# Kernel tuning notes

Hardware: AMD Instinct MI355X
Metric: run time of the kernel (lower is better)

## Reference

```python
import jax, jax.numpy as jnp
import numpy as np
import math

B, C, H, W = 8, 64, 64, 64


def setup_inputs() -> dict:
    key = jax.random.key(0)
    k1, k2, k3, k4 = jax.random.split(key, 4)
    x = jax.random.normal(k1, (B, C, H, W), dtype=jnp.float32)
    fg_mask = jax.random.randint(k2, (B, 1, H, W), 0, 2, dtype=jnp.int32)
    w_qkv = jax.random.normal(k3, (3 * C, C), dtype=jnp.float32) * (1.0 / math.sqrt(C))
    w_proj = jax.random.normal(k4, (C, C), dtype=jnp.float32) * (1.0 / math.sqrt(C))
    b_proj = jnp.zeros((C,), dtype=jnp.float32)
    return {"x": x, "fg_mask": fg_mask, "w_qkv": w_qkv, "w_proj": w_proj, "b_proj": b_proj}


def reference(x, fg_mask, w_qkv, w_proj, b_proj):
    b, c, h, w = x.shape
    n = h * w
    # [B,C,H,W] -> [B,N,C]
    x_flat = x.reshape(b, c, n).transpose(0, 2, 1)
    qkv = x_flat @ w_qkv.T                      # [B,N,3C]
    q, k, v = jnp.split(qkv, 3, axis=-1)        # each [B,N,C]
    attn = jnp.einsum('bnc,bmc->bnm', q, k) / math.sqrt(c)  # [B,N,N]
    fg = fg_mask.reshape(b, n)                  # [B,N]
    attn = jnp.where(fg[:, None, :] == 0, -jnp.inf, attn)
    attn = jax.nn.softmax(attn, axis=-1)
    out = attn @ v                              # [B,N,C]
    out = out @ w_proj.T + b_proj               # [B,N,C]
    return out.transpose(0, 2, 1).reshape(b, c, h, w)
```

## Files before the change

kernel.cpp:

```cpp
#include <hip/hip_runtime.h>
#include <math.h>

#define Bdim 8
#define Cdim 64
#define Ndim 4096
#define TK   32
#define GNT  32

typedef __bf16 bf16x8 __attribute__((ext_vector_type(8)));
typedef __bf16 bf16x4 __attribute__((ext_vector_type(4)));
typedef float  f32x4  __attribute__((ext_vector_type(4)));
typedef float  f32x16 __attribute__((ext_vector_type(16)));

__device__ __forceinline__ void gload_lds16(const void* g, void* l) {
    __builtin_amdgcn_global_load_lds(
        (const __attribute__((address_space(1))) void*)g,
        (__attribute__((address_space(3))) void*)l, 16, 0, 0);
}

__device__ __forceinline__ float fexp2(float x) {
#if __has_builtin(__builtin_amdgcn_exp2f)
    return __builtin_amdgcn_exp2f(x);
#else
    return exp2f(x);
#endif
}

__global__ __launch_bounds__(256) void qkv_mfma_kernel(
    const float* __restrict__ x, const float* __restrict__ w_qkv,
    const int* __restrict__ fg,
    __bf16* __restrict__ Qb, __bf16* __restrict__ Kb, __bf16* __restrict__ Vb,
    float* __restrict__ fgb)
{
    __shared__ __align__(16) __bf16 whs[64 * 64];
    __shared__ __align__(16) __bf16 wls[64 * 64];
    __shared__ __align__(16) __bf16 tr[4][16 * 64];

    const int bx   = blockIdx.x;
    const int jc   = bx % 3;
    const int nblk = (bx / 3) & 63;
    const int b    = bx / 192;
    const int tid  = threadIdx.x;
    const int wv   = tid >> 6;
    const int l    = tid & 63;
    const int g    = l >> 4;
    const int li   = l & 15;
    const int nbase = nblk * 64 + wv * 16;

    const float KS = 0.125f * 1.44269504089f;

    if (jc == 1 && tid < 64) {
        const int n = nblk * 64 + tid;
        fgb[b * Ndim + n] = fg[b * Ndim + n] ? -12.f : -1e30f;
    }

    {
        const float* wsrc = w_qkv + jc * 4096 + tid * 16;
        const float4 f0 = *(const float4*)(wsrc);
        const float4 f1 = *(const float4*)(wsrc + 4);
        const float4 f2 = *(const float4*)(wsrc + 8);
        const float4 f3 = *(const float4*)(wsrc + 12);
        const int row = tid >> 2;
        const int gb  = (tid & 3) * 2;
        bf16x8 h0, l0, h1, l1;
        const float* fp[4] = {(const float*)&f0, (const float*)&f1,
                              (const float*)&f2, (const float*)&f3};
#pragma unroll
        for (int qq = 0; qq < 2; ++qq)
#pragma unroll
            for (int e = 0; e < 8; ++e) {
                const float v = fp[qq * 2 + (e >> 2)][e & 3];
                const __bf16 h = (__bf16)v;
                if (qq == 0) { h0[e] = h; l0[e] = (__bf16)(v - (float)h); }
                else         { h1[e] = h; l1[e] = (__bf16)(v - (float)h); }
            }
        *(bf16x8*)(whs + row * 64 + 8 * ((gb)     ^ (row & 7))) = h0;
        *(bf16x8*)(whs + row * 64 + 8 * ((gb + 1) ^ (row & 7))) = h1;
        *(bf16x8*)(wls + row * 64 + 8 * ((gb)     ^ (row & 7))) = l0;
        *(bf16x8*)(wls + row * 64 + 8 * ((gb + 1) ^ (row & 7))) = l1;
    }

    bf16x8 xhi[2], xlo[2];
#pragma unroll
    for (int kc = 0; kc < 2; ++kc)
#pragma unroll
        for (int jj = 0; jj < 8; ++jj) {
            const int c = kc * 32 + 8 * g + jj;
            const float v = x[((size_t)(b * 64 + c)) * Ndim + nbase + li];
            const __bf16 h = (__bf16)v;
            xhi[kc][jj] = h;
            xlo[kc][jj] = (__bf16)(v - (float)h);
        }
    __syncthreads();

    __bf16* trw = tr[wv];
    const float qs = (jc == 0) ? KS : 1.f;

#pragma unroll
    for (int jt = 0; jt < 4; ++jt) {
        const int rw = 16 * jt + li;
        const int rs = li & 7;
        const bf16x8 ah0 = *(const bf16x8*)(whs + rw * 64 + 8 * (g ^ rs));
        const bf16x8 ah1 = *(const bf16x8*)(whs + rw * 64 + 8 * ((4 + g) ^ rs));
        const bf16x8 al0 = *(const bf16x8*)(wls + rw * 64 + 8 * (g ^ rs));
        const bf16x8 al1 = *(const bf16x8*)(wls + rw * 64 + 8 * ((4 + g) ^ rs));
        f32x4 d = (f32x4){0.f, 0.f, 0.f, 0.f};
        d = __builtin_amdgcn_mfma_f32_16x16x32_bf16(ah0, xhi[0], d, 0, 0, 0);
        d = __builtin_amdgcn_mfma_f32_16x16x32_bf16(ah1, xhi[1], d, 0, 0, 0);
        d = __builtin_amdgcn_mfma_f32_16x16x32_bf16(ah0, xlo[0], d, 0, 0, 0);
        d = __builtin_amdgcn_mfma_f32_16x16x32_bf16(ah1, xlo[1], d, 0, 0, 0);
        d = __builtin_amdgcn_mfma_f32_16x16x32_bf16(al0, xhi[0], d, 0, 0, 0);
        d = __builtin_amdgcn_mfma_f32_16x16x32_bf16(al1, xhi[1], d, 0, 0, 0);

        if (jc == 2) {
#pragma unroll
            for (int r = 0; r < 4; ++r) {
                const int cv = jt * 16 + 4 * g + r;
                Vb[((size_t)(b * 64 + cv)) * Ndim + nbase + li] = (__bf16)d[r];
            }
        } else {
            bf16x4 pk;
#pragma unroll
            for (int r = 0; r < 4; ++r) pk[r] = (__bf16)(d[r] * qs);
            const int gran = (2 * jt + (g >> 1)) ^ (li & 7);
            *(bf16x4*)(trw + li * 64 + gran * 8 + 4 * (g & 1)) = pk;
        }
    }

    if (jc != 2) {
        __bf16* dstm = ((jc == 0) ? Qb : Kb) + ((size_t)b * Ndim + nbase) * 64;
#pragma unroll
        for (int p = 0; p < 2; ++p) {
            const int row = p * 8 + (l >> 3);
            const uint4 vr = *(const uint4*)(
                trw + row * 64 + ((l & 7) ^ (l >> 3)) * 8);
            *(uint4*)(dstm + row * 64 + 8 * (l & 7)) = vr;
        }
    }
}

__global__ __launch_bounds__(512, 4) void attn_kernel(
    const __bf16* __restrict__ Qb, const __bf16* __restrict__ Kb,
    const __bf16* __restrict__ Vb, const float* __restrict__ fgb,
    const float* __restrict__ w_proj, const float* __restrict__ b_proj,
    float* __restrict__ out)
{
    __shared__ __align__(16) __bf16 kt[4][2][TK * 64];
    __shared__ __align__(16) __bf16 vt[4][2][64 * TK];
    __shared__ __align__(16) float  mtf[4][2][TK];

    const int bx   = blockIdx.x;
    const int b    = bx & 7;
    const int qblk = (bx >> 3) & 63;
    const int tid  = threadIdx.x;
    const int wv   = tid >> 6;
    const int grp  = wv >> 1;
    const int wsub = wv & 1;
    const int l    = tid & 63;
    const int q    = l & 31;
    const int hi   = l >> 5;

    const int qrow = qblk * 64 + wsub * 32 + q;
    const __bf16* qbp = Qb + ((size_t)b * Ndim + qrow) * 64;
    bf16x8 qf[4];
#pragma unroll
    for (int s = 0; s < 4; ++s)
        qf[s] = *(const bf16x8*)(qbp + 16 * s + 8 * hi);

    const int kbase0 = grp * 1024;
    const __bf16* ksrcc[2];
    const __bf16* vsrcc[2];
    int kdst[2], vdst[2];
#pragma unroll
    for (int cc = 0; cc < 2; ++cc) {
        const int R  = wsub * 16 + cc * 8 + (l >> 3);
        const int pi = (R & 19) | ((R & 4) << 1) | ((R & 8) >> 1);
        ksrcc[cc] = Kb + ((size_t)b * Ndim + kbase0 + pi) * 64 + 8 * ((l & 7) ^ (R & 7));
        kdst[cc]  = (wsub * 16 + cc * 8) * 64;
        const int row = wsub * 32 + cc * 16 + (l >> 2);
        vsrcc[cc] = Vb + ((size_t)(b * 64 + row)) * Ndim + kbase0
                  + 8 * ((l & 3) ^ ((row >> 1) & 3));
        vdst[cc]  = (wsub * 32 + cc * 16) * TK;
    }
    const float* fgbp = fgb + b * Ndim + kbase0;

    auto stage = [&](int t, int buf) {
#pragma unroll
        for (int cc = 0; cc < 2; ++cc)
            gload_lds16(ksrcc[cc] + (size_t)t * (TK * 64), &kt[grp][buf][kdst[cc]]);
#pragma unroll
        for (int cc = 0; cc < 2; ++cc)
            gload_lds16(vsrcc[cc] + t * TK, &vt[grp][buf][vdst[cc]]);
        if (wsub == 0 && l < 8)
            gload_lds16(fgbp + t * 32 + l * 4, &mtf[grp][buf][0]);
    };

    f32x16 acc0 = {}, acc1 = {};
    f32x4  psv  = {};

    stage(0, 0);

    for (int it = 0; it < GNT; ++it) {
        const int buf = it & 1;
        __syncthreads();
        if (it + 1 < GNT) stage(it + 1, buf ^ 1);

        const float* mrow = &mtf[grp][buf][0];
        const f32x4 ma = *(const f32x4*)(mrow + 8 * hi);
        const f32x4 mb = *(const f32x4*)(mrow + 8 * hi + 4);
        const f32x4 mc = *(const f32x4*)(mrow + 16 + 8 * hi);
        const f32x4 md = *(const f32x4*)(mrow + 20 + 8 * hi);
        f32x16 z;
#pragma unroll
        for (int r = 0; r < 4; ++r) {
            z[r] = ma[r]; z[4 + r] = mb[r]; z[8 + r] = mc[r]; z[12 + r] = md[r];
        }

        __builtin_amdgcn_s_setprio(1);
#pragma unroll
        for (int s = 0; s < 4; ++s) {
            const bf16x8 kf = *(const bf16x8*)(
                &kt[grp][buf][q * 64 + 8 * ((hi + 2 * s) ^ (q & 7))]);
            z = __builtin_amdgcn_mfma_f32_32x32x16_bf16(kf, qf[s], z, 0, 0, 0);
        }
        __builtin_amdgcn_s_setprio(0);

        f32x16 p;
#pragma unroll
        for (int r = 0; r < 16; ++r) {
            p[r] = fexp2(z[r]);
            psv[r & 3] += p[r];
        }
        bf16x8 pb0, pb1;
#pragma unroll
        for (int j = 0; j < 8; ++j) {
            pb0[j] = (__bf16)p[j];
            pb1[j] = (__bf16)p[8 + j];
        }

        __builtin_amdgcn_s_setprio(1);
#pragma unroll
        for (int h = 0; h < 2; ++h) {
            const int c   = 32 * h + q;
            const int csw = (c >> 1) & 3;
            const bf16x8 vf0 = *(const bf16x8*)(&vt[grp][buf][c * 32 + 8 * ((hi)     ^ csw)]);
            const bf16x8 vf1 = *(const bf16x8*)(&vt[grp][buf][c * 32 + 8 * ((hi + 2) ^ csw)]);
            if (h == 0) {
                acc0 = __builtin_amdgcn_mfma_f32_32x32x16_bf16(vf0, pb0, acc0, 0, 0, 0);
                acc0 = __builtin_amdgcn_mfma_f32_32x32x16_bf16(vf1, pb1, acc0, 0, 0, 0);
            } else {
                acc1 = __builtin_amdgcn_mfma_f32_32x32x16_bf16(vf0, pb0, acc1, 0, 0, 0);
                acc1 = __builtin_amdgcn_mfma_f32_32x32x16_bf16(vf1, pb1, acc1, 0, 0, 0);
            }
        }
        __builtin_amdgcn_s_setprio(0);
    }

    float lsum = (psv[0] + psv[1]) + (psv[2] + psv[3]);
    lsum += __shfl_xor(lsum, 32);

    float* mlb = (float*)&kt[0][0][0];
    __syncthreads();

    auto chunk = [&](int cidx) -> float* {
        return (cidx < 4) ? (float*)&vt[0][0][0] + cidx * 2048
                          : mlb + 256 + (cidx - 4) * 2048;
    };

    if (grp > 0) {
        const int pp = grp - 1;
        if (l < 32) mlb[(pp * 2 + wsub) * 32 + l] = lsum;
        float* o = chunk(pp * 2 + wsub);
#pragma unroll
        for (int fi = 0; fi < 8; ++fi) {
            f32x4 v;
#pragma unroll
            for (int e = 0; e < 4; ++e)
                v[e] = (fi < 4) ? acc0[(fi & 3) * 4 + e] : acc1[(fi & 3) * 4 + e];
            *(f32x4*)(o + (fi * 64 + l) * 4) = v;
        }
    }
    __syncthreads();
    if (grp > 0) return;

    float Lt = lsum;
#pragma unroll
    for (int pp = 0; pp < 3; ++pp)
        Lt += mlb[(pp * 2 + wsub) * 32 + q];
    const float inv = 1.f / Lt;

    f32x16 m0 = acc0, m1 = acc1;
#pragma unroll
    for (int pp = 0; pp < 3; ++pp) {
        const float* o = chunk(pp * 2 + wsub);
#pragma unroll
        for (int fi = 0; fi < 8; ++fi) {
            const f32x4 v = *(const f32x4*)(o + (fi * 64 + l) * 4);
#pragma unroll
            for (int e = 0; e < 4; ++e) {
                if (fi < 4) m0[(fi & 3) * 4 + e] += v[e];
                else        m1[(fi & 3) * 4 + e] += v[e];
            }
        }
    }

    bf16x8 ob[4];
#pragma unroll
    for (int s = 0; s < 4; ++s)
#pragma unroll
        for (int j = 0; j < 8; ++j) {
            const float vv = (s < 2) ? m0[j + 8 * (s & 1)] : m1[j + 8 * (s & 1)];
            ob[s][j] = (__bf16)(vv * inv);
        }

    const int nb = qblk * 64 + wsub * 32;
#pragma unroll
    for (int H = 0; H < 2; ++H) {
        const int co = 32 * H + q;
        f32x16 y = {};
#pragma unroll
        for (int s = 0; s < 4; ++s) {
            const float* wr = w_proj + co * 64 + 4 * hi + 16 * s;
            const float4 fA = *(const float4*)(wr);
            const float4 fB = *(const float4*)(wr + 8);
            bf16x8 wf;
            wf[0] = (__bf16)fA.x; wf[1] = (__bf16)fA.y;
            wf[2] = (__bf16)fA.z; wf[3] = (__bf16)fA.w;
            wf[4] = (__bf16)fB.x; wf[5] = (__bf16)fB.y;
            wf[6] = (__bf16)fB.z; wf[7] = (__bf16)fB.w;
            y = __builtin_amdgcn_mfma_f32_32x32x16_bf16(wf, ob[s], y, 0, 0, 0);
        }
#pragma unroll
        for (int rq = 0; rq < 4; ++rq) {
            const f32x4 bp = *(const f32x4*)(b_proj + 32 * H + 4 * hi + 8 * rq);
#pragma unroll
            for (int e = 0; e < 4; ++e) {
                const int co2 = 32 * H + e + 8 * rq + 4 * hi;
                out[((size_t)(b * 64 + co2)) * Ndim + nb + q] = y[rq * 4 + e] + bp[e];
            }
        }
    }
}

extern "C" void kernel_launch(void* const* d_in, const int* in_sizes, int n_in,
                              void* d_out, int out_size, void* d_ws, size_t ws_size,
                              hipStream_t stream) {
    const float* x      = (const float*)d_in[0];
    const int*   fg     = (const int*)d_in[1];
    const float* w_qkv  = (const float*)d_in[2];
    const float* w_proj = (const float*)d_in[3];
    const float* b_proj = (const float*)d_in[4];
    float* out = (float*)d_out;

    const size_t per = (size_t)Bdim * Cdim * Ndim;
    __bf16* Qb  = (__bf16*)d_ws;
    __bf16* Kb  = Qb + per;
    __bf16* Vb  = Kb + per;
    float*  fgb = (float*)(Vb + per);

    qkv_mfma_kernel<<<dim3(Bdim * (Ndim / 64) * 3), dim3(256), 0, stream>>>(
        x, w_qkv, fg, Qb, Kb, Vb, fgb);
    attn_kernel<<<dim3(Bdim * (Ndim / 64)), dim3(512), 0, stream>>>(
        Qb, Kb, Vb, fgb, w_proj, b_proj, out);
}
```

Measured before the change: 62.39 us.

## Split attention keys across two wave groups instead of four

The attention block shrinks from 512 to 256 threads, so each 64-query tile is processed by two key-range groups of 2048 keys each instead of four groups of 1024. Shared memory for K/V staging halves and the cross-group reduction of partial outputs and row sums now merges one partner instead of three. This lowers LDS use and reduction overhead per block and may allow more blocks per CU, but each wave runs twice as many serial loop iterations and there is less parallelism within a block.

```diff
diff --git a/kernel.cpp b/kernel.cpp
--- a/kernel.cpp
+++ b/kernel.cpp
@@ -5,7 +5,7 @@
 #define Cdim 64
 #define Ndim 4096
 #define TK   32
-#define GNT  32
+#define GNT2 64
 
 typedef __bf16 bf16x8 __attribute__((ext_vector_type(8)));
 typedef __bf16 bf16x4 __attribute__((ext_vector_type(4)));
@@ -139,15 +139,15 @@
     }
 }
 
-__global__ __launch_bounds__(512, 4) void attn_kernel(
+__global__ __launch_bounds__(256, 4) void attn_kernel(
     const __bf16* __restrict__ Qb, const __bf16* __restrict__ Kb,
     const __bf16* __restrict__ Vb, const float* __restrict__ fgb,
     const float* __restrict__ w_proj, const float* __restrict__ b_proj,
     float* __restrict__ out)
 {
-    __shared__ __align__(16) __bf16 kt[4][2][TK * 64];
-    __shared__ __align__(16) __bf16 vt[4][2][64 * TK];
-    __shared__ __align__(16) float  mtf[4][2][TK];
+    __shared__ __align__(16) __bf16 kt[2][2][TK * 64];
+    __shared__ __align__(16) __bf16 vt[2][2][64 * TK];
+    __shared__ __align__(16) float  mtf[2][2][TK];
 
     const int bx   = blockIdx.x;
     const int b    = bx & 7;
@@ -167,7 +167,7 @@
     for (int s = 0; s < 4; ++s)
         qf[s] = *(const bf16x8*)(qbp + 16 * s + 8 * hi);
 
-    const int kbase0 = grp * 1024;
+    const int kbase0 = grp * 2048;
     const __bf16* ksrcc[2];
     const __bf16* vsrcc[2];
     int kdst[2], vdst[2];
@@ -200,10 +200,10 @@
 
     stage(0, 0);
 
-    for (int it = 0; it < GNT; ++it) {
+    for (int it = 0; it < GNT2; ++it) {
         const int buf = it & 1;
         __syncthreads();
-        if (it + 1 < GNT) stage(it + 1, buf ^ 1);
+        if (it + 1 < GNT2) stage(it + 1, buf ^ 1);
 
         const float* mrow = &mtf[grp][buf][0];
         const f32x4 ma = *(const f32x4*)(mrow + 8 * hi);
@@ -260,17 +260,12 @@
     lsum += __shfl_xor(lsum, 32);
 
     float* mlb = (float*)&kt[0][0][0];
+    float* chunkbase = (float*)&vt[0][0][0];
     __syncthreads();
 
-    auto chunk = [&](int cidx) -> float* {
-        return (cidx < 4) ? (float*)&vt[0][0][0] + cidx * 2048
-                          : mlb + 256 + (cidx - 4) * 2048;
-    };
-
-    if (grp > 0) {
-        const int pp = grp - 1;
-        if (l < 32) mlb[(pp * 2 + wsub) * 32 + l] = lsum;
-        float* o = chunk(pp * 2 + wsub);
+    if (grp == 1) {
+        if (l < 32) mlb[wsub * 32 + l] = lsum;
+        float* o = chunkbase + wsub * 2048;
 #pragma unroll
         for (int fi = 0; fi < 8; ++fi) {
             f32x4 v;
@@ -281,18 +276,14 @@
         }
     }
     __syncthreads();
-    if (grp > 0) return;
-
-    float Lt = lsum;
-#pragma unroll
-    for (int pp = 0; pp < 3; ++pp)
-        Lt += mlb[(pp * 2 + wsub) * 32 + q];
+    if (grp == 1) return;
+
+    const float Lt  = lsum + mlb[wsub * 32 + q];
     const float inv = 1.f / Lt;
 
     f32x16 m0 = acc0, m1 = acc1;
-#pragma unroll
-    for (int pp = 0; pp < 3; ++pp) {
-        const float* o = chunk(pp * 2 + wsub);
+    {
+        const float* o = chunkbase + wsub * 2048;
 #pragma unroll
         for (int fi = 0; fi < 8; ++fi) {
             const f32x4 v = *(const f32x4*)(o + (fi * 64 + l) * 4);
@@ -360,6 +351,6 @@
 
     qkv_mfma_kernel<<<dim3(Bdim * (Ndim / 64) * 3), dim3(256), 0, stream>>>(
         x, w_qkv, fg, Qb, Kb, Vb, fgb);
-    attn_kernel<<<dim3(Bdim * (Ndim / 64)), dim3(512), 0, stream>>>(
+    attn_kernel<<<dim3(Bdim * (Ndim / 64)), dim3(256), 0, stream>>>(
         Qb, Kb, Vb, fgb, w_proj, b_proj, out);
 }
```

Result: slower. 74.88 us (+20.0%).

## Read V and mask directly from global memory, shrink attention blocks to four waves

Applied to the files above, without the earlier changes.

The attention kernel now uses 256-thread blocks, each handling 32 query rows with four key-split waves, instead of 512-thread blocks of 64 rows. Only K tiles are still staged into LDS via async global-to-LDS loads. V fragments and the foreground mask are loaded directly from global memory into registers, with the mask prefetched one iteration ahead. This cuts LDS footprint and LDS traffic and may raise occupancy. The costs are uncoalesced, strided global reads for V (rows are Ndim apart) and twice as many blocks each redoing the output projection.

```diff
diff --git a/kernel.cpp b/kernel.cpp
--- a/kernel.cpp
+++ b/kernel.cpp
@@ -5,7 +5,7 @@
 #define Cdim 64
 #define Ndim 4096
 #define TK   32
-#define GNT  32
+#define GNT4 32
 
 typedef __bf16 bf16x8 __attribute__((ext_vector_type(8)));
 typedef __bf16 bf16x4 __attribute__((ext_vector_type(4)));
@@ -139,28 +139,24 @@
     }
 }
 
-__global__ __launch_bounds__(512, 4) void attn_kernel(
+__global__ __launch_bounds__(256, 4) void attn_kernel(
     const __bf16* __restrict__ Qb, const __bf16* __restrict__ Kb,
     const __bf16* __restrict__ Vb, const float* __restrict__ fgb,
     const float* __restrict__ w_proj, const float* __restrict__ b_proj,
     float* __restrict__ out)
 {
     __shared__ __align__(16) __bf16 kt[4][2][TK * 64];
-    __shared__ __align__(16) __bf16 vt[4][2][64 * TK];
-    __shared__ __align__(16) float  mtf[4][2][TK];
 
     const int bx   = blockIdx.x;
     const int b    = bx & 7;
-    const int qblk = (bx >> 3) & 63;
+    const int qblk = (bx >> 3) & 127;
     const int tid  = threadIdx.x;
-    const int wv   = tid >> 6;
-    const int grp  = wv >> 1;
-    const int wsub = wv & 1;
+    const int grp  = tid >> 6;
     const int l    = tid & 63;
     const int q    = l & 31;
     const int hi   = l >> 5;
 
-    const int qrow = qblk * 64 + wsub * 32 + q;
+    const int qrow = qblk * 32 + q;
     const __bf16* qbp = Qb + ((size_t)b * Ndim + qrow) * 64;
     bf16x8 qf[4];
 #pragma unroll
@@ -168,48 +164,55 @@
         qf[s] = *(const bf16x8*)(qbp + 16 * s + 8 * hi);
 
     const int kbase0 = grp * 1024;
-    const __bf16* ksrcc[2];
-    const __bf16* vsrcc[2];
-    int kdst[2], vdst[2];
-#pragma unroll
-    for (int cc = 0; cc < 2; ++cc) {
-        const int R  = wsub * 16 + cc * 8 + (l >> 3);
+    const __bf16* ksrcc[4];
+    int kdst[4];
+#pragma unroll
+    for (int cc = 0; cc < 4; ++cc) {
+        const int R  = cc * 8 + (l >> 3);
         const int pi = (R & 19) | ((R & 4) << 1) | ((R & 8) >> 1);
         ksrcc[cc] = Kb + ((size_t)b * Ndim + kbase0 + pi) * 64 + 8 * ((l & 7) ^ (R & 7));
-        kdst[cc]  = (wsub * 16 + cc * 8) * 64;
-        const int row = wsub * 32 + cc * 16 + (l >> 2);
-        vsrcc[cc] = Vb + ((size_t)(b * 64 + row)) * Ndim + kbase0
-                  + 8 * ((l & 3) ^ ((row >> 1) & 3));
-        vdst[cc]  = (wsub * 32 + cc * 16) * TK;
-    }
-    const float* fgbp = fgb + b * Ndim + kbase0;
-
-    auto stage = [&](int t, int buf) {
-#pragma unroll
-        for (int cc = 0; cc < 2; ++cc)
+        kdst[cc]  = cc * 8 * 64;
+    }
+    const float*  fgbp  = fgb + b * Ndim + kbase0;
+    const __bf16* vbase = Vb + ((size_t)(b * 64)) * Ndim + kbase0;
+
+    auto stageK = [&](int t, int buf) {
+#pragma unroll
+        for (int cc = 0; cc < 4; ++cc)
             gload_lds16(ksrcc[cc] + (size_t)t * (TK * 64), &kt[grp][buf][kdst[cc]]);
-#pragma unroll
-        for (int cc = 0; cc < 2; ++cc)
-            gload_lds16(vsrcc[cc] + t * TK, &vt[grp][buf][vdst[cc]]);
-        if (wsub == 0 && l < 8)
-            gload_lds16(fgbp + t * 32 + l * 4, &mtf[grp][buf][0]);
     };
 
     f32x16 acc0 = {}, acc1 = {};
     f32x4  psv  = {};
 
-    stage(0, 0);
-
-    for (int it = 0; it < GNT; ++it) {
+    stageK(0, 0);
+    f32x4 ma = *(const f32x4*)(fgbp + 8 * hi);
+    f32x4 mb = *(const f32x4*)(fgbp + 8 * hi + 4);
+    f32x4 mc = *(const f32x4*)(fgbp + 16 + 8 * hi);
+    f32x4 md = *(const f32x4*)(fgbp + 20 + 8 * hi);
+
+    for (int it = 0; it < GNT4; ++it) {
         const int buf = it & 1;
         __syncthreads();
-        if (it + 1 < GNT) stage(it + 1, buf ^ 1);
-
-        const float* mrow = &mtf[grp][buf][0];
-        const f32x4 ma = *(const f32x4*)(mrow + 8 * hi);
-        const f32x4 mb = *(const f32x4*)(mrow + 8 * hi + 4);
-        const f32x4 mc = *(const f32x4*)(mrow + 16 + 8 * hi);
-        const f32x4 md = *(const f32x4*)(mrow + 20 + 8 * hi);
+        if (it + 1 < GNT4) stageK(it + 1, buf ^ 1);
+
+        const int k0 = it * TK;
+        const __bf16* vc0 = vbase + (size_t)q * Ndim + k0;
+        const __bf16* vc1 = vbase + (size_t)(32 + q) * Ndim + k0;
+        const bf16x8 vA0 = *(const bf16x8*)(vc0 + 8 * hi);
+        const bf16x8 vA1 = *(const bf16x8*)(vc0 + 16 + 8 * hi);
+        const bf16x8 vB0 = *(const bf16x8*)(vc1 + 8 * hi);
+        const bf16x8 vB1 = *(const bf16x8*)(vc1 + 16 + 8 * hi);
+
+        f32x4 na = {}, nb2 = {}, nc = {}, nd = {};
+        if (it + 1 < GNT4) {
+            const float* nf = fgbp + (it + 1) * 32;
+            na  = *(const f32x4*)(nf + 8 * hi);
+            nb2 = *(const f32x4*)(nf + 8 * hi + 4);
+            nc  = *(const f32x4*)(nf + 16 + 8 * hi);
+            nd  = *(const f32x4*)(nf + 20 + 8 * hi);
+        }
+
         f32x16 z;
 #pragma unroll
         for (int r = 0; r < 4; ++r) {
@@ -239,38 +242,25 @@
         }
 
         __builtin_amdgcn_s_setprio(1);
-#pragma unroll
-        for (int h = 0; h < 2; ++h) {
-            const int c   = 32 * h + q;
-            const int csw = (c >> 1) & 3;
-            const bf16x8 vf0 = *(const bf16x8*)(&vt[grp][buf][c * 32 + 8 * ((hi)     ^ csw)]);
-            const bf16x8 vf1 = *(const bf16x8*)(&vt[grp][buf][c * 32 + 8 * ((hi + 2) ^ csw)]);
-            if (h == 0) {
-                acc0 = __builtin_amdgcn_mfma_f32_32x32x16_bf16(vf0, pb0, acc0, 0, 0, 0);
-                acc0 = __builtin_amdgcn_mfma_f32_32x32x16_bf16(vf1, pb1, acc0, 0, 0, 0);
-            } else {
-                acc1 = __builtin_amdgcn_mfma_f32_32x32x16_bf16(vf0, pb0, acc1, 0, 0, 0);
-                acc1 = __builtin_amdgcn_mfma_f32_32x32x16_bf16(vf1, pb1, acc1, 0, 0, 0);
-            }
-        }
+        acc0 = __builtin_amdgcn_mfma_f32_32x32x16_bf16(vA0, pb0, acc0, 0, 0, 0);
+        acc0 = __builtin_amdgcn_mfma_f32_32x32x16_bf16(vA1, pb1, acc0, 0, 0, 0);
+        acc1 = __builtin_amdgcn_mfma_f32_32x32x16_bf16(vB0, pb0, acc1, 0, 0, 0);
+        acc1 = __builtin_amdgcn_mfma_f32_32x32x16_bf16(vB1, pb1, acc1, 0, 0, 0);
         __builtin_amdgcn_s_setprio(0);
+
+        ma = na; mb = nb2; mc = nc; md = nd;
     }
 
     float lsum = (psv[0] + psv[1]) + (psv[2] + psv[3]);
     lsum += __shfl_xor(lsum, 32);
 
-    float* mlb = (float*)&kt[0][0][0];
+    float* mrg = (float*)&kt[0][0][0];
     __syncthreads();
-
-    auto chunk = [&](int cidx) -> float* {
-        return (cidx < 4) ? (float*)&vt[0][0][0] + cidx * 2048
-                          : mlb + 256 + (cidx - 4) * 2048;
-    };
 
     if (grp > 0) {
         const int pp = grp - 1;
-        if (l < 32) mlb[(pp * 2 + wsub) * 32 + l] = lsum;
-        float* o = chunk(pp * 2 + wsub);
+        if (l < 32) mrg[6144 + pp * 32 + l] = lsum;
+        float* o = mrg + pp * 2048;
 #pragma unroll
         for (int fi = 0; fi < 8; ++fi) {
             f32x4 v;
@@ -286,13 +276,13 @@
     float Lt = lsum;
 #pragma unroll
     for (int pp = 0; pp < 3; ++pp)
-        Lt += mlb[(pp * 2 + wsub) * 32 + q];
+        Lt += mrg[6144 + pp * 32 + q];
     const float inv = 1.f / Lt;
 
     f32x16 m0 = acc0, m1 = acc1;
 #pragma unroll
     for (int pp = 0; pp < 3; ++pp) {
-        const float* o = chunk(pp * 2 + wsub);
+        const float* o = mrg + pp * 2048;
 #pragma unroll
         for (int fi = 0; fi < 8; ++fi) {
             const f32x4 v = *(const f32x4*)(o + (fi * 64 + l) * 4);
@@ -313,7 +303,7 @@
             ob[s][j] = (__bf16)(vv * inv);
         }
 
-    const int nb = qblk * 64 + wsub * 32;
+    const int nb = qblk * 32;
 #pragma unroll
     for (int H = 0; H < 2; ++H) {
         const int co = 32 * H + q;
@@ -360,6 +350,6 @@
 
     qkv_mfma_kernel<<<dim3(Bdim * (Ndim / 64) * 3), dim3(256), 0, stream>>>(
         x, w_qkv, fg, Qb, Kb, Vb, fgb);
-    attn_kernel<<<dim3(Bdim * (Ndim / 64)), dim3(512), 0, stream>>>(
+    attn_kernel<<<dim3(Bdim * (Ndim / 32)), dim3(256), 0, stream>>>(
         Qb, Kb, Vb, fgb, w_proj, b_proj, out);
 }
```

After: 138.7 us. 122% more time.
